# Performance work log

Measured on AMD Instinct MI355X. Metric: run time of the kernel, lower is better.

The kernel has to match this reference:

```python
import jax, jax.numpy as jnp
import numpy as np

NINP, NHID, NTOK, NLAYERS, BSZ = 4096, 512, 50257, 2, 32
T_ENC, T_DEC = 80, 40


def lstm_layer(x, h0, c0, Wih, Whh, b):
    """Single LSTM layer over a [T,B,in] sequence; PyTorch gate order i,f,g,o."""
    def step(carry, xt):
        h, c = carry
        z = xt @ Wih.T + h @ Whh.T + b  # [B, 4H]
        i, f, g, o = jnp.split(z, 4, axis=-1)
        c = jax.nn.sigmoid(f) * c + jax.nn.sigmoid(i) * jnp.tanh(g)
        h = jax.nn.sigmoid(o) * jnp.tanh(c)
        return (h, c), h
    (hN, cN), ys = jax.lax.scan(step, (h0, c0), x)
    return ys, hN, cN


def multi_lstm(x, h0, c0, params):
    """Stacked LSTM; params = list of (Wih, Whh, b) per layer."""
    hs, cs = [], []
    y = x
    for l, (Wih, Whh, b) in enumerate(params):
        y, hN, cN = lstm_layer(y, h0[l], c0[l], Wih, Whh, b)
        hs.append(hN); cs.append(cN)
    return y, jnp.stack(hs), jnp.stack(cs)


def setup_inputs():
    key = jax.random.key(0)
    ks = iter(jax.random.split(key, 32))
    def rn(shape, scale=0.05):
        return (jax.random.normal(next(ks), shape, dtype=jnp.float32) * scale)
    H4 = 4 * NHID
    d = {}
    d["inp"] = rn((T_ENC, BSZ, NINP), 1.0)
    for name in ("hid1_h", "hid1_c", "hid2_h", "hid2_c"):
        d[name] = jnp.zeros((NLAYERS, BSZ, NHID), jnp.float32)
    # lstm1: layer0 in=NINP, layer1 in=NHID (b = b_ih + b_hh fused)
    d["l1_Wih0"] = rn((H4, NINP)); d["l1_Whh0"] = rn((H4, NHID)); d["l1_b0"] = rn((H4,))
    d["l1_Wih1"] = rn((H4, NHID)); d["l1_Whh1"] = rn((H4, NHID)); d["l1_b1"] = rn((H4,))
    # lstm2: layer0 in=2*NHID, layer1 in=NHID
    d["l2_Wih0"] = rn((H4, 2 * NHID)); d["l2_Whh0"] = rn((H4, NHID)); d["l2_b0"] = rn((H4,))
    d["l2_Wih1"] = rn((H4, NHID)); d["l2_Whh1"] = rn((H4, NHID)); d["l2_b1"] = rn((H4,))
    d["W_out"] = rn((NTOK, NHID)); d["b_out"] = rn((NTOK,))
    d["W_emb"] = rn((NHID, NTOK)); d["b_emb"] = rn((NHID,))
    d["target_len"] = T_DEC
    return d


def reference(inp, hid1_h, hid1_c, hid2_h, hid2_c,
              l1_Wih0, l1_Whh0, l1_b0, l1_Wih1, l1_Whh1, l1_b1,
              l2_Wih0, l2_Whh0, l2_b0, l2_Wih1, l2_Whh1, l2_b1,
              W_out, b_out, W_emb, b_emb, target_len):
    p1 = [(l1_Wih0, l1_Whh0, l1_b0), (l1_Wih1, l1_Whh1, l1_b1)]
    p2 = [(l2_Wih0, l2_Whh0, l2_b0), (l2_Wih1, l2_Whh1, l2_b1)]
    T, B, ninp = inp.shape
    H = hid1_h.shape[-1]
    # --- encoding stage ---
    out1, h1, c1 = multi_lstm(inp, hid1_h, hid1_c, p1)
    pad_h = jnp.zeros((T, B, H), inp.dtype)
    _, h2, c2 = multi_lstm(jnp.concatenate([pad_h, out1], axis=-1), hid2_h, hid2_c, p2)
    # --- decoding stage ---
    pad_in = jnp.zeros((target_len, B, ninp), inp.dtype)
    out1d, _, _ = multi_lstm(pad_in, h1, c1, p1)
    # vocab2emb(one-hot BOS at index 0) = W_emb[:, 0] + b_emb; never updated in
    # the original loop (variable-name bug), so it is constant over decode steps,
    # making the per-step loop equivalent to one lstm2 scan.
    bos_emb = W_emb[:, 0] + b_emb  # [H]
    bos = jnp.broadcast_to(bos_emb, (target_len, B, H))
    out2d, _, _ = multi_lstm(jnp.concatenate([bos, out1d], axis=-1), h2, c2, p2)
    logits = jnp.einsum('tbh,vh->tbv', out2d, W_out) + b_out  # [T_dec, B, V]
    return jax.nn.log_softmax(logits, axis=-1)
```

## Files before the change

kernel.cpp:

```cpp
#include <hip/hip_runtime.h>
#include <hip/hip_bf16.h>
#include <cstddef>

#define NINP 4096
#define NHID 512
#define G4   2048
#define NTOK 50257
#define BSZ  32
#define T_ENC 80
#define T_DEC 40

typedef __attribute__((ext_vector_type(4))) float  f32x4;
typedef __attribute__((ext_vector_type(4))) __bf16 bf16x4;
typedef __attribute__((ext_vector_type(8))) __bf16 bf16x8;

__device__ __forceinline__ int sw_off(int r, int k) {
    return r * 128 + ((((k >> 3) ^ (r & 7)) << 4) | ((k & 7) << 1));
}
__device__ __forceinline__ int sw512(int r, int k) {
    return r * 1024 + ((((k >> 3) ^ (r & 7)) << 4) | ((k & 7) << 1));
}

__device__ __forceinline__ void split4(const float4& v, bf16x4& h, bf16x4& l) {
    float a0 = v.x, a1 = v.y, a2 = v.z, a3 = v.w;
    __bf16 h0 = (__bf16)a0, h1 = (__bf16)a1, h2 = (__bf16)a2, h3 = (__bf16)a3;
    h[0] = h0; h[1] = h1; h[2] = h2; h[3] = h3;
    l[0] = (__bf16)(a0 - (float)h0);
    l[1] = (__bf16)(a1 - (float)h1);
    l[2] = (__bf16)(a2 - (float)h2);
    l[3] = (__bf16)(a3 - (float)h3);
}

__device__ __forceinline__ bf16x4 hi4(const float4& v) {
    bf16x4 h; h[0] = (__bf16)v.x; h[1] = (__bf16)v.y;
    h[2] = (__bf16)v.z; h[3] = (__bf16)v.w; return h;
}

__device__ __forceinline__ void split8(const float4& a, const float4& b,
                                       bf16x8& h, bf16x8& l) {
    float x[8] = {a.x, a.y, a.z, a.w, b.x, b.y, b.z, b.w};
    #pragma unroll
    for (int i = 0; i < 8; i++) {
        __bf16 hb = (__bf16)x[i];
        h[i] = hb; l[i] = (__bf16)(x[i] - (float)hb);
    }
}

__device__ __forceinline__ bf16x8 to_bf16x8(const float4& a, const float4& b) {
    bf16x8 r;
    r[0]=(__bf16)a.x; r[1]=(__bf16)a.y; r[2]=(__bf16)a.z; r[3]=(__bf16)a.w;
    r[4]=(__bf16)b.x; r[5]=(__bf16)b.y; r[6]=(__bf16)b.z; r[7]=(__bf16)b.w;
    return r;
}

__device__ __forceinline__ void unpack8(const uint4& a, const uint4& b,
                                        bf16x8& h, bf16x8& l) {
    unsigned u[8] = {a.x, a.y, a.z, a.w, b.x, b.y, b.z, b.w};
    union { unsigned short s; __bf16 v; } t;
    #pragma unroll
    for (int i = 0; i < 8; i++) {
        t.s = (unsigned short)(u[i] & 0xffff); h[i] = t.v;
        t.s = (unsigned short)(u[i] >> 16);    l[i] = t.v;
    }
}
__device__ __forceinline__ bf16x8 unpack_hi8(const uint4& a, const uint4& b) {
    unsigned u[8] = {a.x, a.y, a.z, a.w, b.x, b.y, b.z, b.w};
    union { unsigned short s; __bf16 v; } t;
    bf16x8 h;
    #pragma unroll
    for (int i = 0; i < 8; i++) { t.s = (unsigned short)(u[i] & 0xffff); h[i] = t.v; }
    return h;
}

__device__ __forceinline__ unsigned pack_hilo(float x) {
    __bf16 hb = (__bf16)x;
    float hf = (float)hb;
    __bf16 lb = (__bf16)(x - hf);
    union { __bf16 b; unsigned short s; } ch, cl;
    ch.b = hb; cl.b = lb;
    return (unsigned)ch.s | ((unsigned)cl.s << 16);
}

__device__ __forceinline__ float fast_sigmoid(float x) {
    return 1.f / (1.f + __expf(-x));
}
__device__ __forceinline__ float fast_tanh(float x) {
    return 1.f - 2.f / (__expf(2.f * x) + 1.f);
}

__global__ __launch_bounds__(256) void gemm_hilo(
    const float* __restrict__ A, int lda,
    const float* __restrict__ B, int ldb,
    const float* __restrict__ bias,
    float* __restrict__ Z, int ldz,
    int N, int K)
{
    __shared__ __align__(16) char lds[49152];
    const int tid  = threadIdx.x;
    const int bm   = blockIdx.y * 128;
    const int bn   = blockIdx.x * 128;
    const int wave = tid >> 6;
    const int lane = tid & 63;
    const int wm   = (wave >> 1) * 64;
    const int wn   = (wave & 1) * 64;
    const int lr   = lane & 15;
    const int kg   = lane >> 4;

    const int rr = tid >> 4;
    const int kk = (tid & 15) * 4;

    f32x4 acc[4][4] = {};

    for (int k0 = 0; k0 < K; k0 += 64) {
        float4 av[8], bv[8];
        #pragma unroll
        for (int i = 0; i < 8; i++) {
            int r = i * 16 + rr;
            av[i] = *(const float4*)&A[(size_t)(bm + r) * lda + k0 + kk];
            int rb = bn + r;
            if (rb < N)
                bv[i] = *(const float4*)&B[(size_t)rb * ldb + k0 + kk];
            else
                bv[i] = make_float4(0.f, 0.f, 0.f, 0.f);
        }
        __syncthreads();
        #pragma unroll
        for (int i = 0; i < 8; i++) {
            int r = i * 16 + rr;
            int off = sw_off(r, kk);
            bf16x4 h, l;
            split4(av[i], h, l);
            *(bf16x4*)(lds + off)         = h;
            *(bf16x4*)(lds + 16384 + off) = l;
            *(bf16x4*)(lds + 32768 + off) = hi4(bv[i]);
        }
        __syncthreads();
        #pragma unroll
        for (int ks = 0; ks < 2; ks++) {
            bf16x8 ah[4], al[4], bh[4];
            const int kbase = ks * 32 + kg * 8;
            #pragma unroll
            for (int f = 0; f < 4; f++) {
                int offA = sw_off(wm + f * 16 + lr, kbase);
                ah[f] = *(const bf16x8*)(lds + offA);
                al[f] = *(const bf16x8*)(lds + 16384 + offA);
                int offB = sw_off(wn + f * 16 + lr, kbase);
                bh[f] = *(const bf16x8*)(lds + 32768 + offB);
            }
            #pragma unroll
            for (int fm = 0; fm < 4; fm++)
                #pragma unroll
                for (int fn = 0; fn < 4; fn++) {
                    acc[fm][fn] = __builtin_amdgcn_mfma_f32_16x16x32_bf16(
                        ah[fm], bh[fn], acc[fm][fn], 0, 0, 0);
                    acc[fm][fn] = __builtin_amdgcn_mfma_f32_16x16x32_bf16(
                        al[fm], bh[fn], acc[fm][fn], 0, 0, 0);
                }
        }
    }

    #pragma unroll
    for (int fn = 0; fn < 4; fn++) {
        int col = bn + wn + fn * 16 + lr;
        if (col < N) {
            float bb = bias ? bias[col] : 0.f;
            #pragma unroll
            for (int fm = 0; fm < 4; fm++) {
                #pragma unroll
                for (int j = 0; j < 4; j++) {
                    int row = bm + wm + fm * 16 + kg * 4 + j;
                    Z[(size_t)row * ldz + col] = acc[fm][fn][j] + bb;
                }
            }
        }
    }
}

__device__ __forceinline__ void grid_barrier(unsigned* flags, unsigned* gen,
                                             unsigned target)
{
    __syncthreads();
    if (threadIdx.x == 0) {
        __builtin_amdgcn_fence(__ATOMIC_RELEASE, "agent");
        __hip_atomic_store(&flags[blockIdx.x], target, __ATOMIC_RELAXED,
                           __HIP_MEMORY_SCOPE_AGENT);
    }
    if (blockIdx.x == 0) {
        while (__hip_atomic_load(&flags[threadIdx.x], __ATOMIC_RELAXED,
                                 __HIP_MEMORY_SCOPE_AGENT) < target)
            __builtin_amdgcn_s_sleep(1);
        __syncthreads();
        if (threadIdx.x == 0)
            __hip_atomic_store(gen, target, __ATOMIC_RELAXED,
                               __HIP_MEMORY_SCOPE_AGENT);
    }
    if (threadIdx.x == 0) {
        while (__hip_atomic_load(gen, __ATOMIC_RELAXED,
                                 __HIP_MEMORY_SCOPE_AGENT) < target)
            __builtin_amdgcn_s_sleep(1);
        __builtin_amdgcn_fence(__ATOMIC_ACQUIRE, "agent");
    }
    __syncthreads();
}

__global__ __launch_bounds__(256, 1) void fused_scan(
    const float* __restrict__ Zx,
    const float* __restrict__ Whh_0, const float* __restrict__ bias_0,
    const float* __restrict__ Wih_1, const float* __restrict__ Whh_1,
    const float* __restrict__ bias_1,
    const float* __restrict__ Wih_2, const float* __restrict__ Whh_2,
    const float* __restrict__ bias_2e, const float* __restrict__ bias_2d,
    const float* __restrict__ Wih_3, const float* __restrict__ Whh_3,
    const float* __restrict__ bias_3,
    const float* __restrict__ hid1_h, const float* __restrict__ hid1_c,
    const float* __restrict__ hid2_h, const float* __restrict__ hid2_c,
    float* __restrict__ dec3,
    unsigned* hbuf, unsigned* flags, unsigned* gen)
{
    __shared__ __align__(16) char lds[131072];
    float* a_x = (float*)(lds + 32768);

    const int tid  = threadIdx.x;
    const int L    = blockIdx.x >> 6;
    const int bidc = blockIdx.x & 63;
    const int wave = tid >> 6;
    const int lane = tid & 63;
    const int mh   = wave >> 1;
    const int nh   = wave & 1;
    const int lr   = lane & 15;
    const int kg   = lane >> 4;
    const int jcbase = bidc * 8;
    const int bq = tid >> 3;
    const int aq = tid & 7;

    const float* Whh = (L==0)?Whh_0:(L==1)?Whh_1:(L==2)?Whh_2:Whh_3;
    const float* Wih = (L==1)?Wih_1:(L==2)?Wih_2:(L==3)?Wih_3:nullptr;
    const int ld_ih  = (L==2)?1024:512;
    const float* be  = (L==0)?bias_0:(L==1)?bias_1:(L==2)?bias_2e:bias_3;
    const float* bd  = (L==2)?bias_2d:be;
    const float* h0  = ((L<2)?hid1_h:hid2_h) + (L&1)*16384;
    const float* c0  = ((L<2)?hid1_c:hid2_c) + (L&1)*16384;
    unsigned* myb       = hbuf + L*32768;
    const unsigned* xsb = hbuf + (L>0 ? (L-1)*32768 : 0);

    {
        int gate = (bq<8)?0:(bq<16)?2:(bq<24)?1:3;
        int row  = gate*512 + jcbase + (bq&7);
        const float* wr = Whh + (size_t)row * 512;
        #pragma unroll
        for (int jj = 0; jj < 8; jj++) {
            int k = aq*8 + jj*64;
            *(bf16x8*)(lds + 65536 + sw512(bq, k)) =
                to_bf16x8(*(const float4*)(wr+k), *(const float4*)(wr+k+4));
        }
        if (Wih) {
            const float* wr2 = Wih + (size_t)row * ld_ih;
            #pragma unroll
            for (int jj = 0; jj < 8; jj++) {
                int k = aq*8 + jj*64;
                *(bf16x8*)(lds + 98304 + sw512(bq, k)) =
                    to_bf16x8(*(const float4*)(wr2+k), *(const float4*)(wr2+k+4));
            }
        }
    }

    const int n_col = nh*16 + lr;
    const int gate  = (n_col<8)?0:(n_col<16)?2:(n_col<24)?1:3;
    const int col2048 = gate*512 + jcbase + (n_col & 7);
    const float bbe = be[col2048];
    const float bbd = bd[col2048];

    float cc[4] = {0.f, 0.f, 0.f, 0.f};
    if (nh == 1 && lr < 8) {
        #pragma unroll
        for (int j = 0; j < 4; j++)
            cc[j] = c0[(mh*16 + kg*4 + j)*512 + jcbase + lr];
    }
    __syncthreads();

    const int rowA = mh*16 + lr;
    const int rowB = nh*16 + lr;

    for (int tt = 0; tt < 123; ++tt) {
        const int myt = tt - L;
        if (myt >= 0 && myt < 120) {
            uint4 xr[8][2];
            if (L > 0) {
                const unsigned* xs = xsb + (size_t)(myt & 1)*16384 + bq*512;
                #pragma unroll
                for (int jj = 0; jj < 8; jj++) {
                    int k = aq*8 + jj*64;
                    xr[jj][0] = *(const uint4*)(xs + k);
                    xr[jj][1] = *(const uint4*)(xs + k + 4);
                }
            }
            if (myt == 0) {
                const float* hr = h0 + bq*512;
                #pragma unroll
                for (int jj = 0; jj < 8; jj++) {
                    int k = aq*8 + jj*64;
                    bf16x8 H, Lo;
                    split8(*(const float4*)(hr+k), *(const float4*)(hr+k+4), H, Lo);
                    int off = sw512(bq, k);
                    *(bf16x8*)(lds + off)         = H;
                    *(bf16x8*)(lds + 32768 + off) = Lo;
                }
            } else {
                const unsigned* hs = myb + (size_t)((myt-1) & 1)*16384 + bq*512;
                #pragma unroll
                for (int jj = 0; jj < 8; jj++) {
                    int k = aq*8 + jj*64;
                    bf16x8 H, Lo;
                    unpack8(*(const uint4*)(hs+k), *(const uint4*)(hs+k+4), H, Lo);
                    int off = sw512(bq, k);
                    *(bf16x8*)(lds + off)         = H;
                    *(bf16x8*)(lds + 32768 + off) = Lo;
                }
            }
            __syncthreads();

            f32x4 accA = {0.f,0.f,0.f,0.f}, accB = {0.f,0.f,0.f,0.f};
            #pragma unroll
            for (int ks = 0; ks < 16; ++ks) {
                int k = ks*32 + kg*8;
                int offA = sw512(rowA, k);
                int offB = sw512(rowB, k);
                bf16x8 ah = *(const bf16x8*)(lds + offA);
                bf16x8 al = *(const bf16x8*)(lds + 32768 + offA);
                bf16x8 bh = *(const bf16x8*)(lds + 65536 + offB);
                accA = __builtin_amdgcn_mfma_f32_16x16x32_bf16(ah, bh, accA, 0,0,0);
                accB = __builtin_amdgcn_mfma_f32_16x16x32_bf16(al, bh, accB, 0,0,0);
            }
            __syncthreads();

            if (L > 0) {
                #pragma unroll
                for (int jj = 0; jj < 8; jj++) {
                    int k = aq*8 + jj*64;
                    *(bf16x8*)(lds + sw512(bq, k)) = unpack_hi8(xr[jj][0], xr[jj][1]);
                }
                __syncthreads();
                #pragma unroll
                for (int ks = 0; ks < 16; ++ks) {
                    int k = ks*32 + kg*8;
                    bf16x8 ax = *(const bf16x8*)(lds + sw512(rowA, k));
                    bf16x8 bi = *(const bf16x8*)(lds + 98304 + sw512(rowB, k));
                    accA = __builtin_amdgcn_mfma_f32_16x16x32_bf16(ax, bi, accA, 0,0,0);
                }
            }

            const float bbv = (L == 2 && myt >= 80) ? bbd : bbe;
            float z[4];
            #pragma unroll
            for (int j = 0; j < 4; j++) {
                int b = mh*16 + kg*4 + j;
                float zx = (L == 0 && myt < 80)
                    ? Zx[(size_t)myt*(BSZ*G4) + b*G4 + col2048] : 0.f;
                z[j] = accA[j] + accB[j] + bbv + zx;
            }

            if (nh == 0) {
                float zo[4];
                #pragma unroll
                for (int j = 0; j < 4; j++) zo[j] = __shfl_xor(z[j], 8);
                if (lr < 8) {
                    #pragma unroll
                    for (int j = 0; j < 4; j++)
                        a_x[(mh*16 + kg*4 + j)*8 + lr] =
                            fast_sigmoid(z[j]) * fast_tanh(zo[j]);
                }
            }
            __syncthreads();

            if (nh == 1) {
                float cnew[4] = {0.f,0.f,0.f,0.f};
                if (lr < 8) {
                    #pragma unroll
                    for (int j = 0; j < 4; j++) {
                        float av = a_x[(mh*16 + kg*4 + j)*8 + lr];
                        cnew[j] = fast_sigmoid(z[j]) * cc[j] + av;
                        cc[j] = cnew[j];
                    }
                }
                float cfrom[4];
                #pragma unroll
                for (int j = 0; j < 4; j++) cfrom[j] = __shfl_xor(cnew[j], 8);
                if (lr >= 8) {
                    #pragma unroll
                    for (int j = 0; j < 4; j++) {
                        float hn = fast_sigmoid(z[j]) * fast_tanh(cfrom[j]);
                        int b = mh*16 + kg*4 + j;
                        int hcol = jcbase + (lr - 8);
                        if (L == 3 && myt >= 80)
                            dec3[(size_t)(myt-80)*(BSZ*NHID) + b*512 + hcol] = hn;
                        __hip_atomic_store(&myb[(size_t)(myt & 1)*16384 + b*512 + hcol],
                                           pack_hilo(hn), __ATOMIC_RELAXED,
                                           __HIP_MEMORY_SCOPE_AGENT);
                    }
                }
            }
        }
        grid_barrier(flags, gen, (unsigned)tt + 1u);
    }
}

__global__ __launch_bounds__(256) void bias2_kernel(
    const float* __restrict__ W_emb,
    const float* __restrict__ b_emb,
    const float* __restrict__ Wih0,
    const float* __restrict__ b0,
    float* __restrict__ bias2)
{
    __shared__ float bos[NHID];
    const int tid = threadIdx.x;
    for (int i = tid; i < NHID; i += 256)
        bos[i] = W_emb[(size_t)i * NTOK] + b_emb[i];
    __syncthreads();
    int j = blockIdx.x * 256 + tid;
    float acc = b0[j];
    for (int k = 0; k < NHID; k++)
        acc += bos[k] * Wih0[(size_t)j * 1024 + k];
    bias2[j] = acc;
}

__global__ __launch_bounds__(256) void logsoftmax_kernel(float* __restrict__ logits)
{
    const size_t row = blockIdx.x;
    float* p = logits + row * (size_t)NTOK;
    const int tid = threadIdx.x;

    float m = -1e30f, s = 0.f;
    for (int i = tid; i < NTOK; i += 256) {
        float x = p[i];
        float mn = fmaxf(m, x);
        s = s * __expf(m - mn) + __expf(x - mn);
        m = mn;
    }
    #pragma unroll
    for (int off = 32; off > 0; off >>= 1) {
        float mo = __shfl_down(m, off);
        float so = __shfl_down(s, off);
        float mn = fmaxf(m, mo);
        s = s * __expf(m - mn) + so * __expf(mo - mn);
        m = mn;
    }
    __shared__ float sm[4], ss[4];
    if ((tid & 63) == 0) { sm[tid >> 6] = m; ss[tid >> 6] = s; }
    __syncthreads();
    float M4 = fmaxf(fmaxf(sm[0], sm[1]), fmaxf(sm[2], sm[3]));
    float S  = ss[0] * __expf(sm[0] - M4) + ss[1] * __expf(sm[1] - M4)
             + ss[2] * __expf(sm[2] - M4) + ss[3] * __expf(sm[3] - M4);
    float lse = M4 + logf(S);
    for (int i = tid; i < NTOK; i += 256) p[i] = p[i] - lse;
}

extern "C" void kernel_launch(void* const* d_in, const int* in_sizes, int n_in,
                              void* d_out, int out_size, void* d_ws, size_t ws_size,
                              hipStream_t stream)
{
    const float* inp     = (const float*)d_in[0];
    const float* hid1_h  = (const float*)d_in[1];
    const float* hid1_c  = (const float*)d_in[2];
    const float* hid2_h  = (const float*)d_in[3];
    const float* hid2_c  = (const float*)d_in[4];
    const float* l1_Wih0 = (const float*)d_in[5];
    const float* l1_Whh0 = (const float*)d_in[6];
    const float* l1_b0   = (const float*)d_in[7];
    const float* l1_Wih1 = (const float*)d_in[8];
    const float* l1_Whh1 = (const float*)d_in[9];
    const float* l1_b1   = (const float*)d_in[10];
    const float* l2_Wih0 = (const float*)d_in[11];
    const float* l2_Whh0 = (const float*)d_in[12];
    const float* l2_b0   = (const float*)d_in[13];
    const float* l2_Wih1 = (const float*)d_in[14];
    const float* l2_Whh1 = (const float*)d_in[15];
    const float* l2_b1   = (const float*)d_in[16];
    const float* W_out   = (const float*)d_in[17];
    const float* b_out   = (const float*)d_in[18];
    const float* W_emb   = (const float*)d_in[19];
    const float* b_emb   = (const float*)d_in[20];

    float* out = (float*)d_out;
    float* ws  = (float*)d_ws;

    float* Zx    = ws;
    float* dec3  = ws + 5242880;
    float* bias2 = ws + 5898240;
    unsigned* hbuf  = (unsigned*)(ws + 5900288);
    unsigned* flags = (unsigned*)(ws + 6031360);
    unsigned* gen   = flags + 256;

    (void)hipMemsetAsync(flags, 0, 1028, stream);

    {
        dim3 grid((G4 + 127) / 128, (T_ENC * BSZ) / 128);
        gemm_hilo<<<grid, dim3(256), 0, stream>>>(
            inp, NINP, l1_Wih0, NINP, nullptr, Zx, G4, G4, NINP);
    }
    bias2_kernel<<<8, 256, 0, stream>>>(W_emb, b_emb, l2_Wih0, l2_b0, bias2);

    fused_scan<<<256, 256, 0, stream>>>(
        Zx,
        l1_Whh0, l1_b0,
        l1_Wih1, l1_Whh1, l1_b1,
        l2_Wih0 + 512, l2_Whh0, l2_b0, bias2,
        l2_Wih1, l2_Whh1, l2_b1,
        hid1_h, hid1_c, hid2_h, hid2_c,
        dec3, hbuf, flags, gen);

    {
        dim3 grid((NTOK + 127) / 128, (T_DEC * BSZ) / 128);
        gemm_hilo<<<grid, dim3(256), 0, stream>>>(
            dec3, NHID, W_out, NHID, b_out, out, NTOK, NTOK, NHID);
    }
    logsoftmax_kernel<<<1280, dim3(256), 0, stream>>>(out);
}
```

Measured before the change: 2.041 ms.

## Replace grid barrier with per-layer dataflow flags and depth-4 ring buffers

Replaces the global grid barrier in the fused wavefront LSTM scan with point-to-point flag waits. Each layer block group waits only on its own layer's previous step, the layer below's current step, and back-pressure from the layer above. A 4-deep ring of split hi/lo bf16 hidden-state buffers replaces the double buffer, the input x is staged into LDS in the same phase as h, and the output projection switches to a hi-only bf16 GEMM. The aim is to cut barrier latency and let layers run out of lockstep, at the cost of more LDS and reduced precision in the output GEMM.

```diff
diff --git a/kernel.cpp b/kernel.cpp
--- a/kernel.cpp
+++ b/kernel.cpp
@@ -9,6 +9,7 @@
 #define BSZ  32
 #define T_ENC 80
 #define T_DEC 40
+#define DQ   4
 
 typedef __attribute__((ext_vector_type(4))) float  f32x4;
 typedef __attribute__((ext_vector_type(4))) __bf16 bf16x4;
@@ -51,34 +52,6 @@
     r[0]=(__bf16)a.x; r[1]=(__bf16)a.y; r[2]=(__bf16)a.z; r[3]=(__bf16)a.w;
     r[4]=(__bf16)b.x; r[5]=(__bf16)b.y; r[6]=(__bf16)b.z; r[7]=(__bf16)b.w;
     return r;
-}
-
-__device__ __forceinline__ void unpack8(const uint4& a, const uint4& b,
-                                        bf16x8& h, bf16x8& l) {
-    unsigned u[8] = {a.x, a.y, a.z, a.w, b.x, b.y, b.z, b.w};
-    union { unsigned short s; __bf16 v; } t;
-    #pragma unroll
-    for (int i = 0; i < 8; i++) {
-        t.s = (unsigned short)(u[i] & 0xffff); h[i] = t.v;
-        t.s = (unsigned short)(u[i] >> 16);    l[i] = t.v;
-    }
-}
-__device__ __forceinline__ bf16x8 unpack_hi8(const uint4& a, const uint4& b) {
-    unsigned u[8] = {a.x, a.y, a.z, a.w, b.x, b.y, b.z, b.w};
-    union { unsigned short s; __bf16 v; } t;
-    bf16x8 h;
-    #pragma unroll
-    for (int i = 0; i < 8; i++) { t.s = (unsigned short)(u[i] & 0xffff); h[i] = t.v; }
-    return h;
-}
-
-__device__ __forceinline__ unsigned pack_hilo(float x) {
-    __bf16 hb = (__bf16)x;
-    float hf = (float)hb;
-    __bf16 lb = (__bf16)(x - hf);
-    union { __bf16 b; unsigned short s; } ch, cl;
-    ch.b = hb; cl.b = lb;
-    return (unsigned)ch.s | ((unsigned)cl.s << 16);
 }
 
 __device__ __forceinline__ float fast_sigmoid(float x) {
@@ -176,31 +149,84 @@
     }
 }
 
-__device__ __forceinline__ void grid_barrier(unsigned* flags, unsigned* gen,
-                                             unsigned target)
+__global__ __launch_bounds__(256) void gemm_ahi(
+    const float* __restrict__ A, int lda,
+    const float* __restrict__ B, int ldb,
+    const float* __restrict__ bias,
+    float* __restrict__ Z, int ldz,
+    int N, int K)
 {
-    __syncthreads();
-    if (threadIdx.x == 0) {
-        __builtin_amdgcn_fence(__ATOMIC_RELEASE, "agent");
-        __hip_atomic_store(&flags[blockIdx.x], target, __ATOMIC_RELAXED,
-                           __HIP_MEMORY_SCOPE_AGENT);
-    }
-    if (blockIdx.x == 0) {
-        while (__hip_atomic_load(&flags[threadIdx.x], __ATOMIC_RELAXED,
-                                 __HIP_MEMORY_SCOPE_AGENT) < target)
-            __builtin_amdgcn_s_sleep(1);
-        __syncthreads();
-        if (threadIdx.x == 0)
-            __hip_atomic_store(gen, target, __ATOMIC_RELAXED,
-                               __HIP_MEMORY_SCOPE_AGENT);
-    }
-    if (threadIdx.x == 0) {
-        while (__hip_atomic_load(gen, __ATOMIC_RELAXED,
-                                 __HIP_MEMORY_SCOPE_AGENT) < target)
-            __builtin_amdgcn_s_sleep(1);
-        __builtin_amdgcn_fence(__ATOMIC_ACQUIRE, "agent");
-    }
-    __syncthreads();
+    __shared__ __align__(16) char lds[32768];
+    const int tid  = threadIdx.x;
+    const int bm   = blockIdx.y * 128;
+    const int bn   = blockIdx.x * 128;
+    const int wave = tid >> 6;
+    const int lane = tid & 63;
+    const int wm   = (wave >> 1) * 64;
+    const int wn   = (wave & 1) * 64;
+    const int lr   = lane & 15;
+    const int kg   = lane >> 4;
+
+    const int rr = tid >> 4;
+    const int kk = (tid & 15) * 4;
+
+    f32x4 acc[4][4] = {};
+
+    for (int k0 = 0; k0 < K; k0 += 64) {
+        float4 av[8], bv[8];
+        #pragma unroll
+        for (int i = 0; i < 8; i++) {
+            int r = i * 16 + rr;
+            av[i] = *(const float4*)&A[(size_t)(bm + r) * lda + k0 + kk];
+            int rb = bn + r;
+            if (rb < N)
+                bv[i] = *(const float4*)&B[(size_t)rb * ldb + k0 + kk];
+            else
+                bv[i] = make_float4(0.f, 0.f, 0.f, 0.f);
+        }
+        __syncthreads();
+        #pragma unroll
+        for (int i = 0; i < 8; i++) {
+            int r = i * 16 + rr;
+            int off = sw_off(r, kk);
+            *(bf16x4*)(lds + off)         = hi4(av[i]);
+            *(bf16x4*)(lds + 16384 + off) = hi4(bv[i]);
+        }
+        __syncthreads();
+        #pragma unroll
+        for (int ks = 0; ks < 2; ks++) {
+            bf16x8 ah[4], bh[4];
+            const int kbase = ks * 32 + kg * 8;
+            #pragma unroll
+            for (int f = 0; f < 4; f++) {
+                ah[f] = *(const bf16x8*)(lds + sw_off(wm + f * 16 + lr, kbase));
+                bh[f] = *(const bf16x8*)(lds + 16384 + sw_off(wn + f * 16 + lr, kbase));
+            }
+            #pragma unroll
+            for (int fm = 0; fm < 4; fm++)
+                #pragma unroll
+                for (int fn = 0; fn < 4; fn++)
+                    acc[fm][fn] = __builtin_amdgcn_mfma_f32_16x16x32_bf16(
+                        ah[fm], bh[fn], acc[fm][fn], 0, 0, 0);
+        }
+        __syncthreads();
+    }
+
+    #pragma unroll
+    for (int fn = 0; fn < 4; fn++) {
+        int col = bn + wn + fn * 16 + lr;
+        if (col < N) {
+            float bb = bias ? bias[col] : 0.f;
+            #pragma unroll
+            for (int fm = 0; fm < 4; fm++) {
+                #pragma unroll
+                for (int j = 0; j < 4; j++) {
+                    int row = bm + wm + fm * 16 + kg * 4 + j;
+                    Z[(size_t)row * ldz + col] = acc[fm][fn][j] + bb;
+                }
+            }
+        }
+    }
 }
 
 __global__ __launch_bounds__(256, 1) void fused_scan(
@@ -215,10 +241,12 @@
     const float* __restrict__ hid1_h, const float* __restrict__ hid1_c,
     const float* __restrict__ hid2_h, const float* __restrict__ hid2_c,
     float* __restrict__ dec3,
-    unsigned* hbuf, unsigned* flags, unsigned* gen)
+    unsigned short* hip_buf,
+    unsigned short* lop_buf,
+    unsigned* flags)
 {
-    __shared__ __align__(16) char lds[131072];
-    float* a_x = (float*)(lds + 32768);
+    __shared__ __align__(16) char lds[163840];
+    float* a_x = (float*)(lds + 65536);
 
     const int tid  = threadIdx.x;
     const int L    = blockIdx.x >> 6;
@@ -240,8 +268,6 @@
     const float* bd  = (L==2)?bias_2d:be;
     const float* h0  = ((L<2)?hid1_h:hid2_h) + (L&1)*16384;
     const float* c0  = ((L<2)?hid1_c:hid2_c) + (L&1)*16384;
-    unsigned* myb       = hbuf + L*32768;
-    const unsigned* xsb = hbuf + (L>0 ? (L-1)*32768 : 0);
 
     {
         int gate = (bq<8)?0:(bq<16)?2:(bq<24)?1:3;
@@ -250,7 +276,7 @@
         #pragma unroll
         for (int jj = 0; jj < 8; jj++) {
             int k = aq*8 + jj*64;
-            *(bf16x8*)(lds + 65536 + sw512(bq, k)) =
+            *(bf16x8*)(lds + 98304 + sw512(bq, k)) =
                 to_bf16x8(*(const float4*)(wr+k), *(const float4*)(wr+k+4));
         }
         if (Wih) {
@@ -258,7 +284,7 @@
             #pragma unroll
             for (int jj = 0; jj < 8; jj++) {
                 int k = aq*8 + jj*64;
-                *(bf16x8*)(lds + 98304 + sw512(bq, k)) =
+                *(bf16x8*)(lds + 131072 + sw512(bq, k)) =
                     to_bf16x8(*(const float4*)(wr2+k), *(const float4*)(wr2+k+4));
             }
         }
@@ -281,126 +307,145 @@
     const int rowA = mh*16 + lr;
     const int rowB = nh*16 + lr;
 
-    for (int tt = 0; tt < 123; ++tt) {
-        const int myt = tt - L;
-        if (myt >= 0 && myt < 120) {
-            uint4 xr[8][2];
-            if (L > 0) {
-                const unsigned* xs = xsb + (size_t)(myt & 1)*16384 + bq*512;
-                #pragma unroll
-                for (int jj = 0; jj < 8; jj++) {
-                    int k = aq*8 + jj*64;
-                    xr[jj][0] = *(const uint4*)(xs + k);
-                    xr[jj][1] = *(const uint4*)(xs + k + 4);
-                }
-            }
-            if (myt == 0) {
-                const float* hr = h0 + bq*512;
-                #pragma unroll
-                for (int jj = 0; jj < 8; jj++) {
-                    int k = aq*8 + jj*64;
-                    bf16x8 H, Lo;
-                    split8(*(const float4*)(hr+k), *(const float4*)(hr+k+4), H, Lo);
-                    int off = sw512(bq, k);
-                    *(bf16x8*)(lds + off)         = H;
-                    *(bf16x8*)(lds + 32768 + off) = Lo;
-                }
-            } else {
-                const unsigned* hs = myb + (size_t)((myt-1) & 1)*16384 + bq*512;
-                #pragma unroll
-                for (int jj = 0; jj < 8; jj++) {
-                    int k = aq*8 + jj*64;
-                    bf16x8 H, Lo;
-                    unpack8(*(const uint4*)(hs+k), *(const uint4*)(hs+k+4), H, Lo);
-                    int off = sw512(bq, k);
-                    *(bf16x8*)(lds + off)         = H;
-                    *(bf16x8*)(lds + 32768 + off) = Lo;
-                }
-            }
-            __syncthreads();
-
-            f32x4 accA = {0.f,0.f,0.f,0.f}, accB = {0.f,0.f,0.f,0.f};
+    for (int t = 0; t < 120; ++t) {
+        if (wave == 0) {
+            for (;;) {
+                bool ok = true;
+                if (t > 0)
+                    ok &= __hip_atomic_load(&flags[L*64 + lane], __ATOMIC_RELAXED,
+                                            __HIP_MEMORY_SCOPE_AGENT) >= (unsigned)t;
+                if (L > 0)
+                    ok &= __hip_atomic_load(&flags[(L-1)*64 + lane], __ATOMIC_RELAXED,
+                                            __HIP_MEMORY_SCOPE_AGENT) >= (unsigned)(t+1);
+                if (L < 3 && t >= 4)
+                    ok &= __hip_atomic_load(&flags[(L+1)*64 + lane], __ATOMIC_RELAXED,
+                                            __HIP_MEMORY_SCOPE_AGENT) >= (unsigned)(t-3);
+                if (__all(ok)) break;
+            }
+            __builtin_amdgcn_fence(__ATOMIC_ACQUIRE, "agent");
+        }
+        __syncthreads();
+
+        if (t == 0) {
+            const float* hr = h0 + bq*512;
+            #pragma unroll
+            for (int jj = 0; jj < 8; jj++) {
+                int k = aq*8 + jj*64;
+                bf16x8 H, Lo;
+                split8(*(const float4*)(hr+k), *(const float4*)(hr+k+4), H, Lo);
+                int off = sw512(bq, k);
+                *(bf16x8*)(lds + off)         = H;
+                *(bf16x8*)(lds + 32768 + off) = Lo;
+            }
+        } else {
+            const size_t sbase = ((size_t)(L*DQ + ((t-1)&3)))*16384 + bq*512;
+            const unsigned short* hp = hip_buf + sbase;
+            const unsigned short* lp = lop_buf + sbase;
+            #pragma unroll
+            for (int jj = 0; jj < 8; jj++) {
+                int k = aq*8 + jj*64;
+                uint4 hv = *(const uint4*)(hp + k);
+                uint4 lv = *(const uint4*)(lp + k);
+                int off = sw512(bq, k);
+                *(uint4*)(lds + off)         = hv;
+                *(uint4*)(lds + 32768 + off) = lv;
+            }
+        }
+        if (L > 0) {
+            const unsigned short* xp =
+                hip_buf + ((size_t)((L-1)*DQ + (t&3)))*16384 + bq*512;
+            #pragma unroll
+            for (int jj = 0; jj < 8; jj++) {
+                int k = aq*8 + jj*64;
+                *(uint4*)(lds + 65536 + sw512(bq, k)) = *(const uint4*)(xp + k);
+            }
+        }
+        __syncthreads();
+
+        f32x4 accA = {0.f,0.f,0.f,0.f}, accB = {0.f,0.f,0.f,0.f};
+        #pragma unroll
+        for (int ks = 0; ks < 16; ++ks) {
+            int k = ks*32 + kg*8;
+            int offA = sw512(rowA, k);
+            int offB = sw512(rowB, k);
+            bf16x8 ah = *(const bf16x8*)(lds + offA);
+            bf16x8 al = *(const bf16x8*)(lds + 32768 + offA);
+            bf16x8 bh = *(const bf16x8*)(lds + 98304 + offB);
+            accA = __builtin_amdgcn_mfma_f32_16x16x32_bf16(ah, bh, accA, 0,0,0);
+            accB = __builtin_amdgcn_mfma_f32_16x16x32_bf16(al, bh, accB, 0,0,0);
+        }
+        if (L > 0) {
             #pragma unroll
             for (int ks = 0; ks < 16; ++ks) {
                 int k = ks*32 + kg*8;
-                int offA = sw512(rowA, k);
-                int offB = sw512(rowB, k);
-                bf16x8 ah = *(const bf16x8*)(lds + offA);
-                bf16x8 al = *(const bf16x8*)(lds + 32768 + offA);
-                bf16x8 bh = *(const bf16x8*)(lds + 65536 + offB);
-                accA = __builtin_amdgcn_mfma_f32_16x16x32_bf16(ah, bh, accA, 0,0,0);
-                accB = __builtin_amdgcn_mfma_f32_16x16x32_bf16(al, bh, accB, 0,0,0);
-            }
-            __syncthreads();
-
-            if (L > 0) {
-                #pragma unroll
-                for (int jj = 0; jj < 8; jj++) {
-                    int k = aq*8 + jj*64;
-                    *(bf16x8*)(lds + sw512(bq, k)) = unpack_hi8(xr[jj][0], xr[jj][1]);
+                bf16x8 ax = *(const bf16x8*)(lds + 65536 + sw512(rowA, k));
+                bf16x8 bi = *(const bf16x8*)(lds + 131072 + sw512(rowB, k));
+                accA = __builtin_amdgcn_mfma_f32_16x16x32_bf16(ax, bi, accA, 0,0,0);
+            }
+        }
+        __syncthreads();
+
+        const float bbv = (L == 2 && t >= 80) ? bbd : bbe;
+        float z[4];
+        #pragma unroll
+        for (int j = 0; j < 4; j++) {
+            int b = mh*16 + kg*4 + j;
+            float zx = (L == 0 && t < 80)
+                ? Zx[(size_t)t*(BSZ*G4) + b*G4 + col2048] : 0.f;
+            z[j] = accA[j] + accB[j] + bbv + zx;
+        }
+
+        if (nh == 0) {
+            float zo[4];
+            #pragma unroll
+            for (int j = 0; j < 4; j++) zo[j] = __shfl_xor(z[j], 8);
+            if (lr < 8) {
+                #pragma unroll
+                for (int j = 0; j < 4; j++)
+                    a_x[(mh*16 + kg*4 + j)*8 + lr] =
+                        fast_sigmoid(z[j]) * fast_tanh(zo[j]);
+            }
+        }
+        __syncthreads();
+
+        if (nh == 1) {
+            float cnew[4] = {0.f,0.f,0.f,0.f};
+            if (lr < 8) {
+                #pragma unroll
+                for (int j = 0; j < 4; j++) {
+                    float av = a_x[(mh*16 + kg*4 + j)*8 + lr];
+                    cnew[j] = fast_sigmoid(z[j]) * cc[j] + av;
+                    cc[j] = cnew[j];
                 }
-                __syncthreads();
-                #pragma unroll
-                for (int ks = 0; ks < 16; ++ks) {
-                    int k = ks*32 + kg*8;
-                    bf16x8 ax = *(const bf16x8*)(lds + sw512(rowA, k));
-                    bf16x8 bi = *(const bf16x8*)(lds + 98304 + sw512(rowB, k));
-                    accA = __builtin_amdgcn_mfma_f32_16x16x32_bf16(ax, bi, accA, 0,0,0);
+            }
+            float cfrom[4];
+            #pragma unroll
+            for (int j = 0; j < 4; j++) cfrom[j] = __shfl_xor(cnew[j], 8);
+            if (lr >= 8) {
+                const size_t wbase = ((size_t)(L*DQ + (t&3)))*16384;
+                #pragma unroll
+                for (int j = 0; j < 4; j++) {
+                    float hn = fast_sigmoid(z[j]) * fast_tanh(cfrom[j]);
+                    int b = mh*16 + kg*4 + j;
+                    int hcol = jcbase + (lr - 8);
+                    __bf16 hb = (__bf16)hn;
+                    __bf16 lb = (__bf16)(hn - (float)hb);
+                    union { __bf16 v; unsigned short s; } ch, cl;
+                    ch.v = hb; cl.v = lb;
+                    hip_buf[wbase + b*512 + hcol] = ch.s;
+                    lop_buf[wbase + b*512 + hcol] = cl.s;
+                    if (L == 3 && t >= 80)
+                        dec3[(size_t)(t-80)*(BSZ*NHID) + b*512 + hcol] = hn;
                 }
             }
-
-            const float bbv = (L == 2 && myt >= 80) ? bbd : bbe;
-            float z[4];
-            #pragma unroll
-            for (int j = 0; j < 4; j++) {
-                int b = mh*16 + kg*4 + j;
-                float zx = (L == 0 && myt < 80)
-                    ? Zx[(size_t)myt*(BSZ*G4) + b*G4 + col2048] : 0.f;
-                z[j] = accA[j] + accB[j] + bbv + zx;
-            }
-
-            if (nh == 0) {
-                float zo[4];
-                #pragma unroll
-                for (int j = 0; j < 4; j++) zo[j] = __shfl_xor(z[j], 8);
-                if (lr < 8) {
-                    #pragma unroll
-                    for (int j = 0; j < 4; j++)
-                        a_x[(mh*16 + kg*4 + j)*8 + lr] =
-                            fast_sigmoid(z[j]) * fast_tanh(zo[j]);
-                }
-            }
-            __syncthreads();
-
-            if (nh == 1) {
-                float cnew[4] = {0.f,0.f,0.f,0.f};
-                if (lr < 8) {
-                    #pragma unroll
-                    for (int j = 0; j < 4; j++) {
-                        float av = a_x[(mh*16 + kg*4 + j)*8 + lr];
-                        cnew[j] = fast_sigmoid(z[j]) * cc[j] + av;
-                        cc[j] = cnew[j];
-                    }
-                }
-                float cfrom[4];
-                #pragma unroll
-                for (int j = 0; j < 4; j++) cfrom[j] = __shfl_xor(cnew[j], 8);
-                if (lr >= 8) {
-                    #pragma unroll
-                    for (int j = 0; j < 4; j++) {
-                        float hn = fast_sigmoid(z[j]) * fast_tanh(cfrom[j]);
-                        int b = mh*16 + kg*4 + j;
-                        int hcol = jcbase + (lr - 8);
-                        if (L == 3 && myt >= 80)
-                            dec3[(size_t)(myt-80)*(BSZ*NHID) + b*512 + hcol] = hn;
-                        __hip_atomic_store(&myb[(size_t)(myt & 1)*16384 + b*512 + hcol],
-                                           pack_hilo(hn), __ATOMIC_RELAXED,
-                                           __HIP_MEMORY_SCOPE_AGENT);
-                    }
-                }
-            }
-        }
-        grid_barrier(flags, gen, (unsigned)tt + 1u);
+        }
+
+        __syncthreads();
+        if (tid == 0) {
+            __builtin_amdgcn_fence(__ATOMIC_RELEASE, "agent");
+            __hip_atomic_store(&flags[L*64 + bidc], (unsigned)(t+1),
+                               __ATOMIC_RELAXED, __HIP_MEMORY_SCOPE_AGENT);
+        }
     }
 }
 
@@ -486,11 +531,11 @@
     float* Zx    = ws;
     float* dec3  = ws + 5242880;
     float* bias2 = ws + 5898240;
-    unsigned* hbuf  = (unsigned*)(ws + 5900288);
-    unsigned* flags = (unsigned*)(ws + 6031360);
-    unsigned* gen   = flags + 256;
-
-    (void)hipMemsetAsync(flags, 0, 1028, stream);
+    unsigned short* hip_buf = (unsigned short*)(ws + 5900288);
+    unsigned short* lop_buf = (unsigned short*)(ws + 6031360);
+    unsigned* flags = (unsigned*)(ws + 6162432);
+
+    (void)hipMemsetAsync(flags, 0, 1024, stream);
 
     {
         dim3 grid((G4 + 127) / 128, (T_ENC * BSZ) / 128);
@@ -506,11 +551,11 @@
         l2_Wih0 + 512, l2_Whh0, l2_b0, bias2,
         l2_Wih1, l2_Whh1, l2_b1,
         hid1_h, hid1_c, hid2_h, hid2_c,
-        dec3, hbuf, flags, gen);
+        dec3, hip_buf, lop_buf, flags);
 
     {
         dim3 grid((NTOK + 127) / 128, (T_DEC * BSZ) / 128);
-        gemm_hilo<<<grid, dim3(256), 0, stream>>>(
+        gemm_ahi<<<grid, dim3(256), 0, stream>>>(
             dec3, NHID, W_out, NHID, b_out, out, NTOK, NTOK, NHID);
     }
     logsoftmax_kernel<<<1280, dim3(256), 0, stream>>>(out);
```

Measured after the change: 2.444 ms. 19.8% more time.

## Hold recurrent weights in registers, split hi/lo h buffers, add vocab GEMM

Applied to the files above, without the earlier changes.

The fused LSTM scan now keeps each block's Whh and Wih bf16 fragments in registers instead of LDS. Gate columns are interleaved so one lane quartet holds i,f,g,o for a hidden unit, and the gate math runs through lane shuffles instead of an LDS exchange with extra barriers. Hidden states go to separate hi and lo bf16 buffers that are copied straight into LDS without unpacking, and the decoder output is stored as bf16. A new vocab GEMM loads each W_out tile into LDS once and loops over all M tiles with hi-only bf16 activations. The register-resident weights raise register pressure, and dropping the lo part of the decoder activations costs some precision in the logits.

```diff
diff --git a/kernel.cpp b/kernel.cpp
--- a/kernel.cpp
+++ b/kernel.cpp
@@ -16,6 +16,9 @@
 
 __device__ __forceinline__ int sw_off(int r, int k) {
     return r * 128 + ((((k >> 3) ^ (r & 7)) << 4) | ((k & 7) << 1));
+}
+__device__ __forceinline__ int swA(int r, int k) {
+    return r * 256 + ((((k >> 3) ^ (r & 7)) << 4) | ((k & 7) << 1));
 }
 __device__ __forceinline__ int sw512(int r, int k) {
     return r * 1024 + ((((k >> 3) ^ (r & 7)) << 4) | ((k & 7) << 1));
@@ -51,34 +54,6 @@
     r[0]=(__bf16)a.x; r[1]=(__bf16)a.y; r[2]=(__bf16)a.z; r[3]=(__bf16)a.w;
     r[4]=(__bf16)b.x; r[5]=(__bf16)b.y; r[6]=(__bf16)b.z; r[7]=(__bf16)b.w;
     return r;
-}
-
-__device__ __forceinline__ void unpack8(const uint4& a, const uint4& b,
-                                        bf16x8& h, bf16x8& l) {
-    unsigned u[8] = {a.x, a.y, a.z, a.w, b.x, b.y, b.z, b.w};
-    union { unsigned short s; __bf16 v; } t;
-    #pragma unroll
-    for (int i = 0; i < 8; i++) {
-        t.s = (unsigned short)(u[i] & 0xffff); h[i] = t.v;
-        t.s = (unsigned short)(u[i] >> 16);    l[i] = t.v;
-    }
-}
-__device__ __forceinline__ bf16x8 unpack_hi8(const uint4& a, const uint4& b) {
-    unsigned u[8] = {a.x, a.y, a.z, a.w, b.x, b.y, b.z, b.w};
-    union { unsigned short s; __bf16 v; } t;
-    bf16x8 h;
-    #pragma unroll
-    for (int i = 0; i < 8; i++) { t.s = (unsigned short)(u[i] & 0xffff); h[i] = t.v; }
-    return h;
-}
-
-__device__ __forceinline__ unsigned pack_hilo(float x) {
-    __bf16 hb = (__bf16)x;
-    float hf = (float)hb;
-    __bf16 lb = (__bf16)(x - hf);
-    union { __bf16 b; unsigned short s; } ch, cl;
-    ch.b = hb; cl.b = lb;
-    return (unsigned)ch.s | ((unsigned)cl.s << 16);
 }
 
 __device__ __forceinline__ float fast_sigmoid(float x) {
@@ -176,6 +151,96 @@
     }
 }
 
+__global__ __launch_bounds__(256, 1) void gemm_vocab(
+    const __bf16* __restrict__ Ah,
+    const float* __restrict__ B,
+    const float* __restrict__ bias,
+    float* __restrict__ Z)
+{
+    __shared__ __align__(16) char lds[163840];
+    char* ldsB = lds;
+    char* ldsA = lds + 131072;
+
+    const int tid  = threadIdx.x;
+    const int bn   = blockIdx.x * 128;
+    const int wave = tid >> 6;
+    const int lane = tid & 63;
+    const int wm   = (wave >> 1) * 64;
+    const int wn   = (wave & 1) * 64;
+    const int lr   = lane & 15;
+    const int kg   = lane >> 4;
+
+    #pragma unroll 4
+    for (int jj = 0; jj < 32; jj++) {
+        int e = tid + jj * 256;
+        int row = e >> 6;
+        int k = (e & 63) * 8;
+        int gr = bn + row;
+        float4 v0, v1;
+        if (gr < NTOK) {
+            v0 = *(const float4*)&B[(size_t)gr * 512 + k];
+            v1 = *(const float4*)&B[(size_t)gr * 512 + k + 4];
+        } else {
+            v0 = make_float4(0.f,0.f,0.f,0.f); v1 = v0;
+        }
+        *(bf16x8*)(ldsB + sw512(row, k)) = to_bf16x8(v0, v1);
+    }
+
+    float bb[4];
+    #pragma unroll
+    for (int fn = 0; fn < 4; fn++) {
+        int col = bn + wn + fn * 16 + lr;
+        bb[fn] = (col < NTOK) ? bias[col] : 0.f;
+    }
+    __syncthreads();
+
+    for (int mt = 0; mt < 10; mt++) {
+        f32x4 acc[4][4] = {};
+        for (int k0 = 0; k0 < 4; k0++) {
+            __syncthreads();
+            #pragma unroll
+            for (int jj = 0; jj < 8; jj++) {
+                int e = tid + jj * 256;
+                int row = e >> 4;
+                int k = (e & 15) * 8;
+                uint4 v = *(const uint4*)&Ah[(size_t)(mt * 128 + row) * 512 + k0 * 128 + k];
+                *(uint4*)(ldsA + swA(row, k)) = v;
+            }
+            __syncthreads();
+            #pragma unroll
+            for (int ks = 0; ks < 4; ks++) {
+                bf16x8 ah[4], bh[4];
+                const int ka = ks * 32 + kg * 8;
+                #pragma unroll
+                for (int f = 0; f < 4; f++) {
+                    ah[f] = *(const bf16x8*)(ldsA + swA(wm + f * 16 + lr, ka));
+                    bh[f] = *(const bf16x8*)(ldsB + sw512(wn + f * 16 + lr, k0 * 128 + ka));
+                }
+                #pragma unroll
+                for (int fm = 0; fm < 4; fm++)
+                    #pragma unroll
+                    for (int fn = 0; fn < 4; fn++)
+                        acc[fm][fn] = __builtin_amdgcn_mfma_f32_16x16x32_bf16(
+                            ah[fm], bh[fn], acc[fm][fn], 0, 0, 0);
+            }
+        }
+        #pragma unroll
+        for (int fn = 0; fn < 4; fn++) {
+            int col = bn + wn + fn * 16 + lr;
+            if (col < NTOK) {
+                #pragma unroll
+                for (int fm = 0; fm < 4; fm++) {
+                    #pragma unroll
+                    for (int j = 0; j < 4; j++) {
+                        int row = mt * 128 + wm + fm * 16 + kg * 4 + j;
+                        Z[(size_t)row * NTOK + col] = acc[fm][fn][j] + bb[fn];
+                    }
+                }
+            }
+        }
+    }
+}
+
 __device__ __forceinline__ void grid_barrier(unsigned* flags, unsigned* gen,
                                              unsigned target)
 {
@@ -214,11 +279,12 @@
     const float* __restrict__ bias_3,
     const float* __restrict__ hid1_h, const float* __restrict__ hid1_c,
     const float* __restrict__ hid2_h, const float* __restrict__ hid2_c,
-    float* __restrict__ dec3,
-    unsigned* hbuf, unsigned* flags, unsigned* gen)
-{
-    __shared__ __align__(16) char lds[131072];
-    float* a_x = (float*)(lds + 32768);
+    __bf16* __restrict__ dec3h,
+    unsigned short* hip_buf,
+    unsigned short* lop_buf,
+    unsigned* flags, unsigned* gen)
+{
+    __shared__ __align__(16) char lds[98304];
 
     const int tid  = threadIdx.x;
     const int L    = blockIdx.x >> 6;
@@ -226,9 +292,10 @@
     const int wave = tid >> 6;
     const int lane = tid & 63;
     const int mh   = wave >> 1;
-    const int nh   = wave & 1;
+    const int ng   = wave & 1;
     const int lr   = lane & 15;
     const int kg   = lane >> 4;
+    const int lr3  = lr & 3;
     const int jcbase = bidc * 8;
     const int bq = tid >> 3;
     const int aq = tid & 7;
@@ -240,59 +307,50 @@
     const float* bd  = (L==2)?bias_2d:be;
     const float* h0  = ((L<2)?hid1_h:hid2_h) + (L&1)*16384;
     const float* c0  = ((L<2)?hid1_c:hid2_c) + (L&1)*16384;
-    unsigned* myb       = hbuf + L*32768;
-    const unsigned* xsb = hbuf + (L>0 ? (L-1)*32768 : 0);
-
+
+    const int hcol = jcbase + ng*4 + (lr >> 2);
+    const int grow = lr3 * 512 + hcol;
+    const float bbe = be[grow];
+    const float bbd = bd[grow];
+
+    bf16x8 whh_f[16], wih_f[16];
     {
-        int gate = (bq<8)?0:(bq<16)?2:(bq<24)?1:3;
-        int row  = gate*512 + jcbase + (bq&7);
-        const float* wr = Whh + (size_t)row * 512;
+        const float* wr = Whh + (size_t)grow * 512;
         #pragma unroll
-        for (int jj = 0; jj < 8; jj++) {
-            int k = aq*8 + jj*64;
-            *(bf16x8*)(lds + 65536 + sw512(bq, k)) =
-                to_bf16x8(*(const float4*)(wr+k), *(const float4*)(wr+k+4));
-        }
-        if (Wih) {
-            const float* wr2 = Wih + (size_t)row * ld_ih;
-            #pragma unroll
-            for (int jj = 0; jj < 8; jj++) {
-                int k = aq*8 + jj*64;
-                *(bf16x8*)(lds + 98304 + sw512(bq, k)) =
-                    to_bf16x8(*(const float4*)(wr2+k), *(const float4*)(wr2+k+4));
-            }
-        }
-    }
-
-    const int n_col = nh*16 + lr;
-    const int gate  = (n_col<8)?0:(n_col<16)?2:(n_col<24)?1:3;
-    const int col2048 = gate*512 + jcbase + (n_col & 7);
-    const float bbe = be[col2048];
-    const float bbd = bd[col2048];
-
-    float cc[4] = {0.f, 0.f, 0.f, 0.f};
-    if (nh == 1 && lr < 8) {
-        #pragma unroll
-        for (int j = 0; j < 4; j++)
-            cc[j] = c0[(mh*16 + kg*4 + j)*512 + jcbase + lr];
-    }
-    __syncthreads();
+        for (int ks = 0; ks < 16; ks++) {
+            int k = ks * 32 + kg * 8;
+            whh_f[ks] = to_bf16x8(*(const float4*)(wr + k),
+                                  *(const float4*)(wr + k + 4));
+        }
+        if (L > 0) {
+            const float* wr2 = Wih + (size_t)grow * ld_ih;
+            #pragma unroll
+            for (int ks = 0; ks < 16; ks++) {
+                int k = ks * 32 + kg * 8;
+                wih_f[ks] = to_bf16x8(*(const float4*)(wr2 + k),
+                                      *(const float4*)(wr2 + k + 4));
+            }
+        } else {
+            #pragma unroll
+            for (int ks = 0; ks < 16; ks++) wih_f[ks] = bf16x8{};
+        }
+    }
+
+    float cc[4];
+    #pragma unroll
+    for (int j = 0; j < 4; j++)
+        cc[j] = c0[(mh*16 + kg*4 + j)*512 + hcol];
 
     const int rowA = mh*16 + lr;
-    const int rowB = nh*16 + lr;
 
     for (int tt = 0; tt < 123; ++tt) {
         const int myt = tt - L;
         if (myt >= 0 && myt < 120) {
-            uint4 xr[8][2];
-            if (L > 0) {
-                const unsigned* xs = xsb + (size_t)(myt & 1)*16384 + bq*512;
-                #pragma unroll
-                for (int jj = 0; jj < 8; jj++) {
-                    int k = aq*8 + jj*64;
-                    xr[jj][0] = *(const uint4*)(xs + k);
-                    xr[jj][1] = *(const uint4*)(xs + k + 4);
-                }
+            float zx[4] = {0.f, 0.f, 0.f, 0.f};
+            if (L == 0 && myt < 80) {
+                #pragma unroll
+                for (int j = 0; j < 4; j++)
+                    zx[j] = Zx[(size_t)myt*(BSZ*G4) + (mh*16+kg*4+j)*G4 + grow];
             }
             if (myt == 0) {
                 const float* hr = h0 + bq*512;
@@ -306,15 +364,26 @@
                     *(bf16x8*)(lds + 32768 + off) = Lo;
                 }
             } else {
-                const unsigned* hs = myb + (size_t)((myt-1) & 1)*16384 + bq*512;
+                const size_t sb = ((size_t)(L*2 + ((myt-1)&1)))*16384 + bq*512;
+                const unsigned short* hp = hip_buf + sb;
+                const unsigned short* lp = lop_buf + sb;
                 #pragma unroll
                 for (int jj = 0; jj < 8; jj++) {
                     int k = aq*8 + jj*64;
-                    bf16x8 H, Lo;
-                    unpack8(*(const uint4*)(hs+k), *(const uint4*)(hs+k+4), H, Lo);
+                    uint4 hv = *(const uint4*)(hp + k);
+                    uint4 lv = *(const uint4*)(lp + k);
                     int off = sw512(bq, k);
-                    *(bf16x8*)(lds + off)         = H;
-                    *(bf16x8*)(lds + 32768 + off) = Lo;
+                    *(uint4*)(lds + off)         = hv;
+                    *(uint4*)(lds + 32768 + off) = lv;
+                }
+            }
+            if (L > 0) {
+                const unsigned short* xp =
+                    hip_buf + ((size_t)((L-1)*2 + (myt&1)))*16384 + bq*512;
+                #pragma unroll
+                for (int jj = 0; jj < 8; jj++) {
+                    int k = aq*8 + jj*64;
+                    *(uint4*)(lds + 65536 + sw512(bq, k)) = *(const uint4*)(xp + k);
                 }
             }
             __syncthreads();
@@ -324,79 +393,60 @@
             for (int ks = 0; ks < 16; ++ks) {
                 int k = ks*32 + kg*8;
                 int offA = sw512(rowA, k);
-                int offB = sw512(rowB, k);
                 bf16x8 ah = *(const bf16x8*)(lds + offA);
                 bf16x8 al = *(const bf16x8*)(lds + 32768 + offA);
-                bf16x8 bh = *(const bf16x8*)(lds + 65536 + offB);
-                accA = __builtin_amdgcn_mfma_f32_16x16x32_bf16(ah, bh, accA, 0,0,0);
-                accB = __builtin_amdgcn_mfma_f32_16x16x32_bf16(al, bh, accB, 0,0,0);
-            }
-            __syncthreads();
-
+                accA = __builtin_amdgcn_mfma_f32_16x16x32_bf16(ah, whh_f[ks], accA, 0,0,0);
+                accB = __builtin_amdgcn_mfma_f32_16x16x32_bf16(al, whh_f[ks], accB, 0,0,0);
+            }
             if (L > 0) {
-                #pragma unroll
-                for (int jj = 0; jj < 8; jj++) {
-                    int k = aq*8 + jj*64;
-                    *(bf16x8*)(lds + sw512(bq, k)) = unpack_hi8(xr[jj][0], xr[jj][1]);
-                }
-                __syncthreads();
                 #pragma unroll
                 for (int ks = 0; ks < 16; ++ks) {
                     int k = ks*32 + kg*8;
-                    bf16x8 ax = *(const bf16x8*)(lds + sw512(rowA, k));
-                    bf16x8 bi = *(const bf16x8*)(lds + 98304 + sw512(rowB, k));
-                    accA = __builtin_amdgcn_mfma_f32_16x16x32_bf16(ax, bi, accA, 0,0,0);
+                    bf16x8 ax = *(const bf16x8*)(lds + 65536 + sw512(rowA, k));
+                    accA = __builtin_amdgcn_mfma_f32_16x16x32_bf16(ax, wih_f[ks], accA, 0,0,0);
                 }
             }
 
             const float bbv = (L == 2 && myt >= 80) ? bbd : bbe;
-            float z[4];
+            float z[4], t0[4];
             #pragma unroll
             for (int j = 0; j < 4; j++) {
-                int b = mh*16 + kg*4 + j;
-                float zx = (L == 0 && myt < 80)
-                    ? Zx[(size_t)myt*(BSZ*G4) + b*G4 + col2048] : 0.f;
-                z[j] = accA[j] + accB[j] + bbv + zx;
-            }
-
-            if (nh == 0) {
-                float zo[4];
-                #pragma unroll
-                for (int j = 0; j < 4; j++) zo[j] = __shfl_xor(z[j], 8);
-                if (lr < 8) {
-                    #pragma unroll
-                    for (int j = 0; j < 4; j++)
-                        a_x[(mh*16 + kg*4 + j)*8 + lr] =
-                            fast_sigmoid(z[j]) * fast_tanh(zo[j]);
-                }
-            }
-            __syncthreads();
-
-            if (nh == 1) {
-                float cnew[4] = {0.f,0.f,0.f,0.f};
-                if (lr < 8) {
-                    #pragma unroll
-                    for (int j = 0; j < 4; j++) {
-                        float av = a_x[(mh*16 + kg*4 + j)*8 + lr];
-                        cnew[j] = fast_sigmoid(z[j]) * cc[j] + av;
-                        cc[j] = cnew[j];
-                    }
-                }
-                float cfrom[4];
-                #pragma unroll
-                for (int j = 0; j < 4; j++) cfrom[j] = __shfl_xor(cnew[j], 8);
-                if (lr >= 8) {
-                    #pragma unroll
-                    for (int j = 0; j < 4; j++) {
-                        float hn = fast_sigmoid(z[j]) * fast_tanh(cfrom[j]);
-                        int b = mh*16 + kg*4 + j;
-                        int hcol = jcbase + (lr - 8);
-                        if (L == 3 && myt >= 80)
-                            dec3[(size_t)(myt-80)*(BSZ*NHID) + b*512 + hcol] = hn;
-                        __hip_atomic_store(&myb[(size_t)(myt & 1)*16384 + b*512 + hcol],
-                                           pack_hilo(hn), __ATOMIC_RELAXED,
-                                           __HIP_MEMORY_SCOPE_AGENT);
-                    }
+                z[j] = accA[j] + accB[j] + bbv + zx[j];
+                t0[j] = (lr3 == 2) ? fast_tanh(z[j]) : fast_sigmoid(z[j]);
+            }
+            float av[4], cn[4], tc[4], hn[4];
+            #pragma unroll
+            for (int j = 0; j < 4; j++) {
+                float x2 = __shfl_xor(t0[j], 2);
+                av[j] = t0[j] * x2;
+            }
+            #pragma unroll
+            for (int j = 0; j < 4; j++) {
+                float x1 = __shfl_xor(av[j], 1);
+                cn[j] = t0[j] * cc[j] + x1;
+                cc[j] = cn[j];
+                tc[j] = fast_tanh(cn[j]);
+            }
+            #pragma unroll
+            for (int j = 0; j < 4; j++) {
+                float x2b = __shfl_xor(tc[j], 2);
+                hn[j] = t0[j] * x2b;
+            }
+
+            if (lr3 == 3) {
+                const size_t wb = ((size_t)(L*2 + (myt&1)))*16384;
+                #pragma unroll
+                for (int j = 0; j < 4; j++) {
+                    int b = mh*16 + kg*4 + j;
+                    float v = hn[j];
+                    __bf16 hb = (__bf16)v;
+                    __bf16 lb = (__bf16)(v - (float)hb);
+                    union { __bf16 x; unsigned short s; } ch, cl;
+                    ch.x = hb; cl.x = lb;
+                    hip_buf[wb + b*512 + hcol] = ch.s;
+                    lop_buf[wb + b*512 + hcol] = cl.s;
+                    if (L == 3 && myt >= 80)
+                        dec3h[(size_t)(myt-80)*(BSZ*NHID) + b*512 + hcol] = hb;
                 }
             }
         }
@@ -484,10 +534,11 @@
     float* ws  = (float*)d_ws;
 
     float* Zx    = ws;
-    float* dec3  = ws + 5242880;
-    float* bias2 = ws + 5898240;
-    unsigned* hbuf  = (unsigned*)(ws + 5900288);
-    unsigned* flags = (unsigned*)(ws + 6031360);
+    float* bias2 = ws + 5242880;
+    __bf16* dec3h = (__bf16*)(ws + 5244928);
+    unsigned short* hip_buf = (unsigned short*)(ws + 5572608);
+    unsigned short* lop_buf = (unsigned short*)(ws + 5638144);
+    unsigned* flags = (unsigned*)(ws + 5703680);
     unsigned* gen   = flags + 256;
 
     (void)hipMemsetAsync(flags, 0, 1028, stream);
@@ -506,12 +557,9 @@
         l2_Wih0 + 512, l2_Whh0, l2_b0, bias2,
         l2_Wih1, l2_Whh1, l2_b1,
         hid1_h, hid1_c, hid2_h, hid2_c,
-        dec3, hbuf, flags, gen);
-
-    {
-        dim3 grid((NTOK + 127) / 128, (T_DEC * BSZ) / 128);
-        gemm_hilo<<<grid, dim3(256), 0, stream>>>(
-            dec3, NHID, W_out, NHID, b_out, out, NTOK, NTOK, NHID);
-    }
+        dec3h, hip_buf, lop_buf, flags, gen);
+
+    gemm_vocab<<<(NTOK + 127) / 128, dim3(256), 0, stream>>>(
+        dec3h, W_out, b_out, out);
     logsoftmax_kernel<<<1280, dim3(256), 0, stream>>>(out);
 }
```

New measurement: 2.475 ms. 1.21x slower.
